# Kernel tuning notes

Hardware: AMD Instinct MI355X
Metric: run time of the kernel (lower is better)

The kernel has to match this reference:

```python
import jax, jax.numpy as jnp
import numpy as np

BN_EPS = 1e-5


def setup_inputs() -> dict:
    key = jax.random.key(0)
    ks = jax.random.split(key, 10)
    d = {}
    # EEG-style input: [B, 1, T, electrodes]
    d["x"] = jax.random.normal(ks[0], (512, 1, 1125, 5), dtype=jnp.float32)
    # conv_time: Conv2d(1, 40, (25, 1)) with bias
    d["conv_time_w"] = jax.random.normal(ks[1], (40, 1, 25, 1), dtype=jnp.float32) * 0.05
    d["conv_time_b"] = jax.random.normal(ks[2], (40,), dtype=jnp.float32) * 0.05
    # conv_spat: Conv2d(40, 40, (1, 5), bias=False)
    d["conv_spat_w"] = jax.random.normal(ks[3], (40, 40, 1, 5), dtype=jnp.float32) * 0.05
    # BatchNorm2d(40), eval mode (running stats)
    d["bn_gamma"] = jnp.ones((40,), jnp.float32)
    d["bn_beta"] = jnp.zeros((40,), jnp.float32)
    d["bn_mean"] = jnp.zeros((40,), jnp.float32)
    d["bn_var"] = jnp.ones((40,), jnp.float32)
    # LSTM(input=40, hidden=10): torch layout W_ih [4H, in], W_hh [4H, H]
    d["w_ih"] = jax.random.normal(ks[4], (40, 40), dtype=jnp.float32) * 0.1
    d["w_hh"] = jax.random.normal(ks[5], (40, 10), dtype=jnp.float32) * 0.1
    d["b_ih"] = jax.random.normal(ks[6], (40,), dtype=jnp.float32) * 0.1
    d["b_hh"] = jax.random.normal(ks[7], (40,), dtype=jnp.float32) * 0.1
    # classifier: Linear(10, 2)
    d["fc_w"] = jax.random.normal(ks[8], (2, 10), dtype=jnp.float32) * 0.1
    d["fc_b"] = jnp.zeros((2,), jnp.float32)
    return d


def reference(x, conv_time_w, conv_time_b, conv_spat_w,
              bn_gamma, bn_beta, bn_mean, bn_var,
              w_ih, w_hh, b_ih, b_hh, fc_w, fc_b):
    dn = ("NCHW", "OIHW", "NCHW")
    # conv over time: [B,1,T,5] -> [B,40,T-24,5]
    h = jax.lax.conv_general_dilated(x, conv_time_w, (1, 1), "VALID", dimension_numbers=dn)
    h = h + conv_time_b[None, :, None, None]
    # conv over electrodes: [B,40,T-24,5] -> [B,40,T-24,1]
    h = jax.lax.conv_general_dilated(h, conv_spat_w, (1, 1), "VALID", dimension_numbers=dn)
    # BatchNorm2d (eval, running stats)
    scale = bn_gamma / jnp.sqrt(bn_var + BN_EPS)
    h = h * scale[None, :, None, None] + (bn_beta - bn_mean * scale)[None, :, None, None]
    # AvgPool2d kernel (25,1) stride (5,1): -> [B,40,L,1], L = (T-24-25)//5 + 1
    h = jax.lax.reduce_window(h, 0.0, jax.lax.add, (1, 1, 25, 1), (1, 1, 5, 1), "VALID") / 25.0
    # Dropout2d in eval mode = identity
    # squeeze width + transpose(1,2): [B,40,L] -> [B,L,40]
    h = jnp.transpose(h[..., 0], (0, 2, 1))
    B = h.shape[0]
    H = w_hh.shape[1]  # hidden = 10
    # precompute input-to-gate projection for all timesteps: [L, B, 4H]
    xg = jnp.einsum("blf,gf->lbg", h, w_ih) + b_ih + b_hh

    def step(carry, xt):
        h_prev, c_prev = carry
        gates = xt + h_prev @ w_hh.T          # [B, 4H]
        i, f, g, o = jnp.split(gates, 4, axis=-1)
        i = jax.nn.sigmoid(i)
        f = jax.nn.sigmoid(f)
        g = jnp.tanh(g)
        o = jax.nn.sigmoid(o)
        c = f * c_prev + i * g
        hn = o * jnp.tanh(c)
        return (hn, c), None

    init = (jnp.zeros((B, H), h.dtype), jnp.zeros((B, H), h.dtype))
    (h_last, _), _ = jax.lax.scan(step, init, xg)  # return_seq=False -> last hidden
    return h_last @ fc_w.T + fc_b  # [B, 2]
```

## Files before the change

### kernel.cpp

```cpp
#include <hip/hip_runtime.h>

#define LOG2E 1.44269504088896340736f

typedef float v2f __attribute__((ext_vector_type(2)));

__device__ __forceinline__ float bf2f(unsigned short u) {
    union { unsigned u32; float f; } v; v.u32 = ((unsigned)u) << 16; return v.f;
}
__device__ __forceinline__ unsigned short f2bf(float f) {
    union { float f; unsigned u32; } v; v.f = f;
    unsigned r = (v.u32 + 0x7FFFu + ((v.u32 >> 16) & 1u)) >> 16;
    return (unsigned short)r;
}
__device__ __forceinline__ bool probe_bf16(const void* gma) {
    return *(const unsigned int*)gma == 0x3F803F80u;
}
__device__ __forceinline__ float ldmix(const void* p, int i, bool bf) {
    return bf ? bf2f(((const unsigned short*)p)[i]) : ((const float*)p)[i];
}
__device__ __forceinline__ float dpp_shl(float x, const int n) {
    int r;
    if (n == 1)      r = __builtin_amdgcn_update_dpp(0, __float_as_int(x), 0x101, 0xF, 0xF, true);
    else if (n == 2) r = __builtin_amdgcn_update_dpp(0, __float_as_int(x), 0x102, 0xF, 0xF, true);
    else             r = __builtin_amdgcn_update_dpp(0, __float_as_int(x), 0x103, 0xF, 0xF, true);
    return __int_as_float(r);
}
#if __has_builtin(__builtin_amdgcn_exp2f)
__device__ __forceinline__ float fexp2(float x) { return __builtin_amdgcn_exp2f(x); }
#else
__device__ __forceinline__ float fexp2(float x) {
    float r; asm("v_exp_f32 %0, %1" : "=v"(r) : "v"(x)); return r;
}
#endif

__global__ __launch_bounds__(1024) void prep_kernel(
    const void* __restrict__ ctw,
    const void* __restrict__ ctb,
    const void* __restrict__ csw,
    const void* __restrict__ gma,
    const void* __restrict__ bta,
    const void* __restrict__ mea,
    const void* __restrict__ var,
    const void* __restrict__ wih,
    const void* __restrict__ bih,
    const void* __restrict__ bhh,
    float* __restrict__ Wg,
    float* __restrict__ Bg)
{
    __shared__ float s_wt[1000];
    __shared__ float s_bt[40];
    __shared__ float s_sp[8000];
    __shared__ float s_wih[1600];
    __shared__ float s_scale[40], s_shift[40];
    __shared__ float s_Wc[5000];
    __shared__ float s_P[5200];
    __shared__ float s_Bc[40];
    __shared__ float s_Wp[9920];

    const int t = threadIdx.x;
    const bool bf = probe_bf16(gma);

    for (int i = t; i < 1000; i += 1024) s_wt[i] = ldmix(ctw, i, bf);
    for (int i = t; i < 8000; i += 1024) s_sp[i] = ldmix(csw, i, bf);
    for (int i = t; i < 1600; i += 1024) s_wih[i] = ldmix(wih, i, bf);
    if (t < 40) {
        s_bt[t] = ldmix(ctb, t, bf);
        float sc = ldmix(gma, t, bf) * rsqrtf(ldmix(var, t, bf) + 1e-5f);
        s_scale[t] = sc;
        s_shift[t] = ldmix(bta, t, bf) - ldmix(mea, t, bf) * sc;
    }
    __syncthreads();

    if (t < 200) {
        const int oc = t / 5, kq = (t % 5) * 5;
        float acc[5][5];
        #pragma unroll
        for (int q = 0; q < 5; ++q)
            #pragma unroll
            for (int e = 0; e < 5; ++e) acc[q][e] = 0.f;
        for (int ic = 0; ic < 40; ++ic) {
            float wtv[5], spv[5];
            #pragma unroll
            for (int q = 0; q < 5; ++q) wtv[q] = s_wt[ic * 25 + kq + q];
            #pragma unroll
            for (int e = 0; e < 5; ++e) spv[e] = s_sp[(oc * 40 + ic) * 5 + e];
            #pragma unroll
            for (int q = 0; q < 5; ++q)
                #pragma unroll
                for (int e = 0; e < 5; ++e) acc[q][e] = fmaf(wtv[q], spv[e], acc[q][e]);
        }
        const float sc = s_scale[oc];
        #pragma unroll
        for (int q = 0; q < 5; ++q)
            #pragma unroll
            for (int e = 0; e < 5; ++e)
                s_Wc[(oc * 25 + kq + q) * 5 + e] = acc[q][e] * sc;
    }
    if (t >= 512 && t < 552) {
        const int oc = t - 512;
        float a = 0.f;
        for (int ic = 0; ic < 40; ++ic) {
            float se = 0.f;
            #pragma unroll
            for (int e = 0; e < 5; ++e) se += s_sp[(oc * 40 + ic) * 5 + e];
            a = fmaf(se, s_bt[ic], a);
        }
        s_Bc[oc] = a * s_scale[oc] + s_shift[oc];
    }
    __syncthreads();

    if (t < 200) {
        const int oc = t / 5, e = t % 5;
        float run = 0.f;
        s_P[oc * 130 + e] = 0.f;
        for (int k = 0; k < 25; ++k) {
            run += s_Wc[(oc * 25 + k) * 5 + e];
            s_P[oc * 130 + (k + 1) * 5 + e] = run;
        }
    }
    __syncthreads();

    for (int i = t; i < 9800; i += 1024) {
        const int oc = i / 245, rem = i % 245, j = rem / 5, e = rem % 5;
        const int lo = j - 24 > 0 ? j - 24 : 0;
        const int hi = j < 24 ? j : 24;
        float val = (s_P[oc * 130 + (hi + 1) * 5 + e] - s_P[oc * 130 + lo * 5 + e]) * 0.04f;
        s_Wp[oc * 248 + rem] = val;
    }
    if (t < 120) s_Wp[(t / 3) * 248 + 245 + (t % 3)] = 0.f;
    __syncthreads();

    if (t < 620) {
        const int gp = t / 31, ko = t % 31;
        const int g0 = 2 * gp, kf0 = 8 * ko;
        float acc0[8], acc1[8];
        #pragma unroll
        for (int q = 0; q < 8; ++q) { acc0[q] = 0.f; acc1[q] = 0.f; }
        for (int oc = 0; oc < 40; ++oc) {
            const float4 pa = *reinterpret_cast<const float4*>(&s_Wp[oc * 248 + kf0]);
            const float4 pb = *reinterpret_cast<const float4*>(&s_Wp[oc * 248 + kf0 + 4]);
            const float wa = s_wih[g0 * 40 + oc];
            const float wb = s_wih[(g0 + 1) * 40 + oc];
            acc0[0] = fmaf(wa, pa.x, acc0[0]); acc0[1] = fmaf(wa, pa.y, acc0[1]);
            acc0[2] = fmaf(wa, pa.z, acc0[2]); acc0[3] = fmaf(wa, pa.w, acc0[3]);
            acc0[4] = fmaf(wa, pb.x, acc0[4]); acc0[5] = fmaf(wa, pb.y, acc0[5]);
            acc0[6] = fmaf(wa, pb.z, acc0[6]); acc0[7] = fmaf(wa, pb.w, acc0[7]);
            acc1[0] = fmaf(wb, pa.x, acc1[0]); acc1[1] = fmaf(wb, pa.y, acc1[1]);
            acc1[2] = fmaf(wb, pa.z, acc1[2]); acc1[3] = fmaf(wb, pa.w, acc1[3]);
            acc1[4] = fmaf(wb, pb.x, acc1[4]); acc1[5] = fmaf(wb, pb.y, acc1[5]);
            acc1[6] = fmaf(wb, pb.z, acc1[6]); acc1[7] = fmaf(wb, pb.w, acc1[7]);
        }
        #pragma unroll
        for (int q = 0; q < 8; ++q) {
            Wg[g0 * 248 + kf0 + q]       = acc0[q];
            Wg[(g0 + 1) * 248 + kf0 + q] = acc1[q];
        }
    }
    if (t >= 640 && t < 680) {
        const int g = t - 640;
        float a = ldmix(bih, g, bf) + ldmix(bhh, g, bf);
        for (int oc = 0; oc < 40; ++oc) a = fmaf(s_wih[g * 40 + oc], s_Bc[oc], a);
        Bg[g] = a;
    }
}

__global__ __launch_bounds__(256, 2) void fused_kernel(
    const void* __restrict__ x,
    const float* __restrict__ Wg,
    const float* __restrict__ Bg,
    const void* __restrict__ whh_p,
    const void* __restrict__ fcw_p,
    const void* __restrict__ fcb_p,
    const void* __restrict__ gma,
    void* __restrict__ out)
{
    __shared__ float sw[9920];
    __shared__ float u[8960];

    const int b   = blockIdx.x;
    const int tid = threadIdx.x;
    const bool bf = probe_bf16(gma);

    for (int i = tid; i < 9920; i += 256) sw[i] = Wg[i];
    if (bf) {
        const unsigned short* xp = (const unsigned short*)x + b * 5625;
        for (int i = tid; i < 5625; i += 256) u[i] = bf2f(xp[i]);
    } else {
        const float* xp = (const float*)x + b * 5625;
        for (int i = tid; i < 5625; i += 256) u[i] = xp[i];
    }
    for (int i = 5625 + tid; i < 6144; i += 256) u[i] = 0.f;
    for (int i = 8640 + tid; i < 8960; i += 256) u[i] = 0.f;
    __syncthreads();

    const int wave  = __builtin_amdgcn_readfirstlane(tid >> 6);
    const int lane  = tid & 63;
    const int gb    = 20 * (wave & 1);
    const int lbase = 108 * (wave >> 1);
    const int l0 = lbase + lane;
    const int l1 = l0 + 64;
    const int a0 = 25 * l0, a1 = 25 * l1;

    v2f acc[20];
    #pragma unroll
    for (int gi = 0; gi < 20; ++gi) {
        float bgv = Bg[gb + gi];
        acc[gi] = (v2f){bgv, bgv};
    }

    const int wrow = gb * 248;
    for (int k = 0; k < 248; k += 4) {
        v2f xv0 = (v2f){ u[a0 + k],     u[a1 + k]     };
        v2f xv1 = (v2f){ u[a0 + k + 1], u[a1 + k + 1] };
        v2f xv2 = (v2f){ u[a0 + k + 2], u[a1 + k + 2] };
        v2f xv3 = (v2f){ u[a0 + k + 3], u[a1 + k + 3] };
        #pragma unroll
        for (int gi = 0; gi < 20; ++gi) {
            const float4 w = *reinterpret_cast<const float4*>(&sw[wrow + gi * 248 + k]);
            acc[gi] += xv0 * w.x;
            acc[gi] += xv1 * w.y;
            acc[gi] += xv2 * w.z;
            acc[gi] += xv3 * w.w;
        }
    }
    __syncthreads();

    #pragma unroll
    for (int gi = 0; gi < 20; ++gi) {
        u[l0 * 40 + gb + gi] = acc[gi].x;
        if (lane < 44) u[l1 * 40 + gb + gi] = acc[gi].y;
    }
    __syncthreads();

    if (wave != 0) return;

    const int j   = lane >> 2;
    const int jt  = lane & 3;
    const int jj  = j < 10 ? j : 9;
    const int gl  = 10 * jt + jj;

    const float L2   = 2.0f * LOG2E;
    const float kmul = (jt == 2) ?  L2 : -LOG2E;
    const float aact = (jt == 2) ? -2.0f : (jt == 0 ? L2 : 1.0f);
    const float bact = (jt == 2) ?  1.0f : 0.0f;

    float whhr[10];
    #pragma unroll
    for (int m = 0; m < 10; ++m) whhr[m] = kmul * ldmix(whh_p, gl * 10 + m, bf);

    float xb[6];
    #pragma unroll
    for (int p = 0; p < 6; ++p) xb[p] = kmul * u[p * 40 + gl];

    float cs = 0.f, h = 0.f;

    for (int l = 0; l < 216; l += 6) {
        #pragma unroll
        for (int s = 0; s < 6; ++s) {
            float xv = xb[s];
            xb[s] = kmul * u[(l + s + 6) * 40 + gl];
            float a_ = xv, b_ = 0.f;
            #pragma unroll
            for (int m = 0; m < 10; m += 2) {
                float h0 = __int_as_float(__builtin_amdgcn_readlane(__float_as_int(h), 4 * m));
                float h1 = __int_as_float(__builtin_amdgcn_readlane(__float_as_int(h), 4 * (m + 1)));
                a_ = fmaf(whhr[m], h0, a_);
                b_ = fmaf(whhr[m + 1], h1, b_);
            }
            float accg = a_ + b_;
            float tt  = fexp2(accg);
            float rr  = __builtin_amdgcn_rcpf(1.0f + tt);
            float act = fmaf(aact, rr, bact);
            float fv = dpp_shl(act, 1);
            float gv = dpp_shl(act, 2);
            float ov = dpp_shl(act, 3);
            cs = fmaf(fv, cs, act * gv);
            float t2 = fexp2(cs);
            float r2 = __builtin_amdgcn_rcpf(1.0f + t2);
            float th = fmaf(-2.0f, r2, 1.0f);
            h = ov * th;
        }
    }

    float w0[10], w1[10];
    #pragma unroll
    for (int m = 0; m < 10; ++m) {
        w0[m] = ldmix(fcw_p, m, bf);
        w1[m] = ldmix(fcw_p, 10 + m, bf);
    }
    float o0 = ldmix(fcb_p, 0, bf), o1 = ldmix(fcb_p, 1, bf);
    #pragma unroll
    for (int m = 0; m < 10; ++m) {
        float hm = __int_as_float(__builtin_amdgcn_readlane(__float_as_int(h), 4 * m));
        o0 = fmaf(w0[m], hm, o0);
        o1 = fmaf(w1[m], hm, o1);
    }
    if (lane == 0) {
        if (bf) {
            ((unsigned short*)out)[b * 2]     = f2bf(o0);
            ((unsigned short*)out)[b * 2 + 1] = f2bf(o1);
        } else {
            ((float*)out)[b * 2]     = o0;
            ((float*)out)[b * 2 + 1] = o1;
        }
    }
}

extern "C" void kernel_launch(void* const* d_in, const int* in_sizes, int n_in,
                              void* d_out, int out_size, void* d_ws, size_t ws_size,
                              hipStream_t stream) {
    const void* x    = d_in[0];
    const void* ctw  = d_in[1];
    const void* ctb  = d_in[2];
    const void* csw  = d_in[3];
    const void* gma  = d_in[4];
    const void* bta  = d_in[5];
    const void* mea  = d_in[6];
    const void* var  = d_in[7];
    const void* wih  = d_in[8];
    const void* whh  = d_in[9];
    const void* bih  = d_in[10];
    const void* bhh  = d_in[11];
    const void* fcw  = d_in[12];
    const void* fcb  = d_in[13];

    char* ws = (char*)d_ws;
    float* Wg = (float*)ws;
    float* Bg = (float*)(ws + 40 * 248 * 4);

    prep_kernel<<<1, 1024, 0, stream>>>(ctw, ctb, csw, gma, bta, mea, var,
                                        wih, bih, bhh, Wg, Bg);
    fused_kernel<<<512, 256, 0, stream>>>(x, Wg, Bg, whh, fcw, fcb, gma, d_out);
}
```

Baseline: 163.6 us.

## Split fused kernel into conv-projection kernel and packed LSTM kernel via workspace

Splits the single fused per-batch kernel in two. The first kernel computes the folded conv/BN/pool/input projection into a global gate buffer. The second runs the LSTM recurrence with four batch elements per block, one per wavefront, so the serial recurrence no longer ties up a whole 256-thread block per sample. This adds a global round trip of roughly 18 MB for the gate buffer and an extra launch, and it falls back to the fused kernel when the workspace is too small.

```diff
diff --git a/kernel.cpp b/kernel.cpp
--- a/kernel.cpp
+++ b/kernel.cpp
@@ -164,6 +164,179 @@
     }
 }
 
+__global__ __launch_bounds__(256, 2) void conv_kernel(
+    const void* __restrict__ x,
+    const float* __restrict__ Wg,
+    const float* __restrict__ Bg,
+    const void* __restrict__ gma,
+    float* __restrict__ xg)
+{
+    __shared__ float sw[9920];
+    __shared__ float u[9184];
+
+    const int b   = blockIdx.x;
+    const int tid = threadIdx.x;
+    const bool bf = probe_bf16(gma);
+
+    for (int i = tid; i < 9920; i += 256) sw[i] = Wg[i];
+    if (bf) {
+        const unsigned short* xp = (const unsigned short*)x + b * 5625;
+        for (int i = tid; i < 5625; i += 256) u[i] = bf2f(xp[i]);
+    } else {
+        const float* xp = (const float*)x + b * 5625;
+        for (int i = tid; i < 5625; i += 256) u[i] = xp[i];
+    }
+    for (int i = 5625 + tid; i < 6144; i += 256) u[i] = 0.f;
+    __syncthreads();
+
+    const int wave  = __builtin_amdgcn_readfirstlane(tid >> 6);
+    const int lane  = tid & 63;
+    const int gb    = 20 * (wave & 1);
+    const int lbase = 108 * (wave >> 1);
+    const int l0 = lbase + lane;
+    const int l1 = l0 + 64;
+    const int a0 = 25 * l0, a1 = 25 * l1;
+
+    v2f acc[20];
+    #pragma unroll
+    for (int gi = 0; gi < 20; ++gi) {
+        float bgv = Bg[gb + gi];
+        acc[gi] = (v2f){bgv, bgv};
+    }
+
+    const int wrow = gb * 248;
+    for (int k = 0; k < 248; k += 4) {
+        v2f xv0 = (v2f){ u[a0 + k],     u[a1 + k]     };
+        v2f xv1 = (v2f){ u[a0 + k + 1], u[a1 + k + 1] };
+        v2f xv2 = (v2f){ u[a0 + k + 2], u[a1 + k + 2] };
+        v2f xv3 = (v2f){ u[a0 + k + 3], u[a1 + k + 3] };
+        #pragma unroll
+        for (int gi = 0; gi < 20; ++gi) {
+            const float4 w = *reinterpret_cast<const float4*>(&sw[wrow + gi * 248 + k]);
+            acc[gi] += xv0 * w.x;
+            acc[gi] += xv1 * w.y;
+            acc[gi] += xv2 * w.z;
+            acc[gi] += xv3 * w.w;
+        }
+    }
+    __syncthreads();
+
+    for (int i = 8856 + tid; i < 9184; i += 256) u[i] = 0.f;
+    #pragma unroll
+    for (int gi = 0; gi < 20; ++gi) {
+        const int g = gb + gi;
+        const int t = g / 10, q = g - 10 * t;
+        const int p = 4 * q + t;
+        const float km = (t == 2) ? 2.0f * LOG2E : -LOG2E;
+        u[l0 * 41 + p] = km * acc[gi].x;
+        if (lane < 44) u[l1 * 41 + p] = km * acc[gi].y;
+    }
+    __syncthreads();
+
+    float* dst = xg + b * 8960;
+    for (int i = tid; i < 8960; i += 256)
+        dst[i] = u[(i / 40) * 41 + (i % 40)];
+}
+
+__global__ __launch_bounds__(256) void lstm_kernel(
+    const float* __restrict__ xg,
+    const void* __restrict__ whh_p,
+    const void* __restrict__ fcw_p,
+    const void* __restrict__ fcb_p,
+    const void* __restrict__ gma,
+    void* __restrict__ out)
+{
+    const int tid  = threadIdx.x;
+    const int wave = __builtin_amdgcn_readfirstlane(tid >> 6);
+    const int lane = tid & 63;
+    const int b    = blockIdx.x * 4 + wave;
+    const bool bf  = probe_bf16(gma);
+
+    const int m  = lane < 40 ? lane : 39;
+    const int j  = m >> 2;
+    const int t  = m & 3;
+    const int gl = 10 * t + j;
+
+    const float L2   = 2.0f * LOG2E;
+    const float kmul = (t == 2) ?  L2 : -LOG2E;
+    const float aact = (t == 2) ? -2.0f : (t == 0 ? L2 : 1.0f);
+    const float bact = (t == 2) ?  1.0f : 0.0f;
+
+    float whhr[10];
+    #pragma unroll
+    for (int mm = 0; mm < 10; ++mm) whhr[mm] = kmul * ldmix(whh_p, gl * 10 + mm, bf);
+
+    const float* xp = xg + b * 8960 + m;
+    float xb[6];
+    #pragma unroll
+    for (int p = 0; p < 6; ++p) xb[p] = xp[p * 40];
+
+    float cs = 0.f, h = 0.f;
+
+    for (int l = 0; l < 216; l += 6) {
+        #pragma unroll
+        for (int s = 0; s < 6; ++s) {
+            float xv = xb[s];
+            xb[s] = xp[(l + s + 6) * 40];
+            float h0 = __int_as_float(__builtin_amdgcn_readlane(__float_as_int(h), 0));
+            float h1 = __int_as_float(__builtin_amdgcn_readlane(__float_as_int(h), 4));
+            float h2 = __int_as_float(__builtin_amdgcn_readlane(__float_as_int(h), 8));
+            float h3 = __int_as_float(__builtin_amdgcn_readlane(__float_as_int(h), 12));
+            float h4 = __int_as_float(__builtin_amdgcn_readlane(__float_as_int(h), 16));
+            float h5 = __int_as_float(__builtin_amdgcn_readlane(__float_as_int(h), 20));
+            float h6 = __int_as_float(__builtin_amdgcn_readlane(__float_as_int(h), 24));
+            float h7 = __int_as_float(__builtin_amdgcn_readlane(__float_as_int(h), 28));
+            float h8 = __int_as_float(__builtin_amdgcn_readlane(__float_as_int(h), 32));
+            float h9 = __int_as_float(__builtin_amdgcn_readlane(__float_as_int(h), 36));
+            float a_ = fmaf(whhr[0], h0, xv);
+            a_ = fmaf(whhr[1], h1, a_);
+            a_ = fmaf(whhr[2], h2, a_);
+            float b_ = whhr[3] * h3;
+            b_ = fmaf(whhr[4], h4, b_);
+            b_ = fmaf(whhr[5], h5, b_);
+            float c_ = whhr[6] * h6;
+            c_ = fmaf(whhr[7], h7, c_);
+            float d_ = whhr[8] * h8;
+            d_ = fmaf(whhr[9], h9, d_);
+            float accg = (a_ + b_) + (c_ + d_);
+            float tt  = fexp2(accg);
+            float rr  = __builtin_amdgcn_rcpf(1.0f + tt);
+            float act = fmaf(aact, rr, bact);
+            float fv = dpp_shl(act, 1);
+            float gv = dpp_shl(act, 2);
+            float ov = dpp_shl(act, 3);
+            cs = fmaf(fv, cs, act * gv);
+            float t2 = fexp2(cs);
+            float r2 = __builtin_amdgcn_rcpf(1.0f + t2);
+            float th = fmaf(-2.0f, r2, 1.0f);
+            h = ov * th;
+        }
+    }
+
+    float w0[10], w1[10];
+    #pragma unroll
+    for (int mm = 0; mm < 10; ++mm) {
+        w0[mm] = ldmix(fcw_p, mm, bf);
+        w1[mm] = ldmix(fcw_p, 10 + mm, bf);
+    }
+    float o0 = ldmix(fcb_p, 0, bf), o1 = ldmix(fcb_p, 1, bf);
+    #pragma unroll
+    for (int mm = 0; mm < 10; ++mm) {
+        float hm = __int_as_float(__builtin_amdgcn_readlane(__float_as_int(h), 4 * mm));
+        o0 = fmaf(w0[mm], hm, o0);
+        o1 = fmaf(w1[mm], hm, o1);
+    }
+    if (lane == 0) {
+        if (bf) {
+            ((unsigned short*)out)[b * 2]     = f2bf(o0);
+            ((unsigned short*)out)[b * 2 + 1] = f2bf(o1);
+        } else {
+            ((float*)out)[b * 2]     = o0;
+            ((float*)out)[b * 2 + 1] = o1;
+        }
+    }
+}
+
 __global__ __launch_bounds__(256, 2) void fused_kernel(
     const void* __restrict__ x,
     const float* __restrict__ Wg,
@@ -327,8 +500,16 @@
     char* ws = (char*)d_ws;
     float* Wg = (float*)ws;
     float* Bg = (float*)(ws + 40 * 248 * 4);
+    float* xg = (float*)(ws + 40960);
+
+    const size_t need = 40960u + 512u * 224u * 40u * 4u;
 
     prep_kernel<<<1, 1024, 0, stream>>>(ctw, ctb, csw, gma, bta, mea, var,
                                         wih, bih, bhh, Wg, Bg);
-    fused_kernel<<<512, 256, 0, stream>>>(x, Wg, Bg, whh, fcw, fcb, gma, d_out);
-}
+    if (ws_size >= need) {
+        conv_kernel<<<512, 256, 0, stream>>>(x, Wg, Bg, gma, xg);
+        lstm_kernel<<<128, 256, 0, stream>>>(xg, whh, fcw, fcb, gma, d_out);
+    } else {
+        fused_kernel<<<512, 256, 0, stream>>>(x, Wg, Bg, whh, fcw, fcb, gma, d_out);
+    }
+}
```

Measured after the change: 166.8 us. About the same (+2.0%).
